# Optimization experiments

Hardware: AMD Instinct MI355X
Metric: run time of the kernel (lower is better)

## Reference

```python
import jax, jax.numpy as jnp
import numpy as np

B, N, T, C, H, HH, ED, HOR, OC = 16, 307, 12, 2, 64, 64, 8, 12, 1


def setup_inputs() -> dict:
    key = jax.random.key(0)
    ks = jax.random.split(key, 23)
    r = lambda i, shape: jax.random.normal(ks[i], shape, dtype=jnp.float32) * 0.1
    return dict(
        coeff_a=r(0, (B, N, T - 1, C)), coeff_b=r(1, (B, N, T - 1, C)),
        coeff_c=r(2, (B, N, T - 1, C)), coeff_d=r(3, (B, N, T - 1, C)),
        times=jnp.arange(T, dtype=jnp.float32),
        h_W=r(4, (C, H)), h_b=r(5, (H,)),
        z_W=r(6, (C, H)), z_b=r(7, (H,)),
        f_W_in=r(8, (H, HH)), f_b_in=r(9, (HH,)),
        f_W_mid=r(10, (HH, HH)), f_b_mid=r(11, (HH,)),
        f_W_out=r(12, (HH, H * C)), f_b_out=r(13, (H * C,)),
        g_W_in=r(14, (H, HH)), g_b_in=r(15, (HH,)),
        g_E=r(16, (N, ED)), g_Wpool=r(17, (ED, 2, HH, HH)), g_bpool=r(18, (ED, HH)),
        g_W_out=r(19, (HH, H * H)), g_b_out=r(20, (H * H,)),
        conv_W=r(21, (HOR * OC, H)), conv_b=r(22, (HOR * OC,)),
    )


def _forward(coeff_a, coeff_b, coeff_c, coeff_d, times,
             h_W, h_b, z_W, z_b,
             f_W_in, f_b_in, f_W_mid, f_b_mid, f_W_out, f_b_out,
             g_W_in, g_b_in, g_E, g_Wpool, g_bpool, g_W_out, g_b_out,
             conv_W, conv_b):
    n_int = times.shape[0] - 1

    def spline_deriv(t):
        # natural cubic spline derivative: b + (two_c + three_d*frac)*frac on interval idx
        idx = jnp.clip(jnp.searchsorted(times, t, side='right') - 1, 0, n_int - 1)
        frac = t - times[idx]
        bb = jnp.take(coeff_b, idx, axis=2)
        cc = jnp.take(coeff_c, idx, axis=2)
        dd = jnp.take(coeff_d, idx, axis=2)
        return bb + (cc + dd * frac) * frac  # (B,N,C)

    def func_f(h):
        x = jax.nn.relu(h @ f_W_in + f_b_in)
        x = jax.nn.relu(x @ f_W_mid + f_b_mid)
        x = (x @ f_W_out + f_b_out).reshape(*x.shape[:-1], H, C)
        return jnp.tanh(x)  # (B,N,H,C)

    # adaptive adjacency (constant across time, depends only on node embeddings)
    A = jax.nn.softmax(jax.nn.relu(g_E @ g_E.T), axis=1)       # (N,N)
    supports = jnp.stack([jnp.eye(N, dtype=A.dtype), A])       # (K=2,N,N)
    agc_W = jnp.einsum('nd,dkio->nkio', g_E, g_Wpool)          # (N,K,HH,HH)
    agc_b = g_E @ g_bpool                                      # (N,HH)

    def func_g(z):
        x = jax.nn.relu(z @ g_W_in + g_b_in)                   # (B,N,HH)
        x_g = jnp.einsum('knm,bmc->bnkc', supports, x)         # (B,N,K,HH)
        x = jnp.einsum('bnki,nkio->bno', x_g, agc_W) + agc_b   # (B,N,HH)
        x = jax.nn.relu(x)
        x = (x @ g_W_out + g_b_out).reshape(*x.shape[:-1], H, H)
        return jnp.tanh(x)  # (B,N,H,H)

    def vf(t, h, z):
        dX = spline_deriv(t)                                   # (B,N,C)
        f_v = func_f(h)                                        # (B,N,H,C)
        g_v = func_g(z)                                        # (B,N,H,H)
        dh = jnp.einsum('bnhc,bnc->bnh', f_v, dX)
        fg = jnp.einsum('bnij,bnjc->bnic', g_v, f_v)           # (B,N,H,C)
        dz = jnp.einsum('bnhc,bnc->bnh', fg, dX)
        return dh, dz

    # initial states from spline value at times[0] (= coeff_a at interval 0, frac 0)
    x0 = coeff_a[:, :, 0, :]                                   # (B,N,C)
    h0 = x0 @ h_W + h_b
    z0 = x0 @ z_W + z_b

    def step(carry, ts):
        h, z = carry
        t0, t1 = ts
        dt = t1 - t0
        k1h, k1z = vf(t0, h, z)
        k2h, k2z = vf(t0 + dt / 2, h + dt / 2 * k1h, z + dt / 2 * k1z)
        k3h, k3z = vf(t0 + dt / 2, h + dt / 2 * k2h, z + dt / 2 * k2z)
        k4h, k4z = vf(t1, h + dt * k3h, z + dt * k3z)
        h = h + dt / 6 * (k1h + 2 * k2h + 2 * k3h + k4h)
        z = z + dt / 6 * (k1z + 2 * k2z + 2 * k3z + k4z)
        return (h, z), None

    (hT, zT), _ = jax.lax.scan(step, (h0, z0), (times[:-1], times[1:]))

    # end_conv: Conv2d(1, HOR*OC, kernel=(1,H)) over (B,1,N,H) == linear over H
    out = jnp.einsum('bnh,oh->bon', zT, conv_W) + conv_b[None, :, None]  # (B,HOR*OC,N)
    out = out.reshape(B, HOR, OC, N).transpose(0, 1, 3, 2)               # (B,HOR,N,OC)
    return out


def reference(coeff_a, coeff_b, coeff_c, coeff_d, times,
              h_W, h_b, z_W, z_b,
              f_W_in, f_b_in, f_W_mid, f_b_mid, f_W_out, f_b_out,
              g_W_in, g_b_in, g_E, g_Wpool, g_bpool, g_W_out, g_b_out,
              conv_W, conv_b):
    return _forward(coeff_a, coeff_b, coeff_c, coeff_d, times,
                    h_W, h_b, z_W, z_b,
                    f_W_in, f_b_in, f_W_mid, f_b_mid, f_W_out, f_b_out,
                    g_W_in, g_b_in, g_E, g_Wpool, g_bpool, g_W_out, g_b_out,
                    conv_W, conv_b)
```

## Files before the change

kernel.cpp:

```cpp
#include <hip/hip_runtime.h>

#define NB 16
#define NN 307
#define NI 11

typedef __attribute__((ext_vector_type(8))) short bf16x8;
typedef __attribute__((ext_vector_type(4))) float f32x4;

#define OFF_ABF    0u
#define OFF_AGCWT  51200u
#define OFF_AGCB   1308672u
#define OFF_WT     1329152u
#define OFF_H      1460224u
#define OFF_Z      1774592u
#define OFF_KH     2088960u
#define OFF_KZ     2403328u
#define OFF_ACCH   2717696u
#define OFF_ACCZ   3032064u
#define OFF_XBF    3346432u
#define OFF_XGBF   3510272u
#define OFF_XT     3674112u
#define OFF_YBF    3837952u

__device__ __forceinline__ float tanh_fast(float x){
    float e = __expf(2.0f * x);
    return 1.0f - 2.0f * __builtin_amdgcn_rcpf(e + 1.0f);
}
__device__ __forceinline__ unsigned short f2bf(float f){
    unsigned u = __builtin_bit_cast(unsigned, f);
    unsigned r = u + 0x7FFFu + ((u >> 16) & 1u);
    return (unsigned short)(r >> 16);
}


__global__ void kA(const float* __restrict__ gE, unsigned short* __restrict__ Abf){
    int n = blockIdx.x;
    int lane = threadIdx.x;
    if (n >= NN){
#pragma unroll
        for (int ii = 0; ii < 5; ii++) Abf[n*320 + lane + 64*ii] = 0;
        return;
    }
    float en[8];
#pragma unroll
    for (int d = 0; d < 8; d++) en[d] = gE[n*8 + d];
    float vals[5];
    float mx = -1e30f;
#pragma unroll
    for (int ii = 0; ii < 5; ii++){
        int m = lane + 64*ii;
        float v = -1e30f;
        if (m < NN){
            float a = 0.f;
#pragma unroll
            for (int d = 0; d < 8; d++) a += en[d] * gE[m*8 + d];
            v = fmaxf(a, 0.f);
        }
        vals[ii] = v;
        mx = fmaxf(mx, v);
    }
#pragma unroll
    for (int off = 32; off >= 1; off >>= 1) mx = fmaxf(mx, __shfl_xor(mx, off, 64));
    float s = 0.f;
#pragma unroll
    for (int ii = 0; ii < 5; ii++){
        int m = lane + 64*ii;
        if (m < NN){ vals[ii] = __expf(vals[ii] - mx); s += vals[ii]; }
    }
#pragma unroll
    for (int off = 32; off >= 1; off >>= 1) s += __shfl_xor(s, off, 64);
    float inv = 1.f / s;
#pragma unroll
    for (int ii = 0; ii < 5; ii++){
        int m = lane + 64*ii;
        unsigned short v = 0;
        if (m < NN) v = f2bf(vals[ii] * inv);
        Abf[n*320 + m] = v;
    }
}

__global__ __launch_bounds__(256) void kAgcWT(const float* __restrict__ gE,
                                              const float* __restrict__ gWpool,
                                              unsigned short* __restrict__ agcWt){
    __shared__ float t[128*65];
    int tid = threadIdx.x;
    int n = blockIdx.x;
    float ge[8];
#pragma unroll
    for (int d = 0; d < 8; d++) ge[d] = gE[n*8 + d];
    for (int it = 0; it < 32; it++){
        int e = it*256 + tid;
        int o = e & 63, i = (e >> 6) & 63, kk = e >> 12;
        float acc = 0.f;
#pragma unroll
        for (int d = 0; d < 8; d++) acc += ge[d] * gWpool[((size_t)(d*2 + kk)*64 + i)*64 + o];
        t[(kk*64 + i)*65 + o] = acc;
    }
    __syncthreads();
    for (int it = 0; it < 32; it++){
        int e = it*256 + tid;
        int k = e & 127, o = e >> 7;
        agcWt[((size_t)n*64 + o)*128 + k] = f2bf(t[k*65 + o]);
    }
}

__global__ void kAgcB(const float* __restrict__ gE, const float* __restrict__ gbpool,
                      float* __restrict__ agcb){
    int gid = blockIdx.x*256 + threadIdx.x;
    if (gid >= NN*64) return;
    int o = gid & 63;
    int n = gid >> 6;
    float acc = 0.f;
#pragma unroll
    for (int d = 0; d < 8; d++) acc += gE[n*8 + d] * gbpool[d*64 + o];
    agcb[gid] = acc;
}

__global__ __launch_bounds__(256) void kWt(const float* __restrict__ WgOut,
                                           unsigned short* __restrict__ Wt_sw){
    __shared__ float t[64*65];
    int tid = threadIdx.x;
    int c0 = blockIdx.x*64;
    for (int it = 0; it < 16; it++){
        int e = it*256 + tid;
        int k = e >> 6, c = e & 63;
        t[k*65 + c] = WgOut[(size_t)k*4096 + c0 + c];
    }
    __syncthreads();
    for (int it = 0; it < 16; it++){
        int e = it*256 + tid;
        int c = e >> 6, k = e & 63;
        int ks = ((((k >> 3) ^ (c & 7)) << 3) | (k & 7));
        Wt_sw[(size_t)(c0 + c)*64 + ks] = f2bf(t[k*65 + c]);
    }
}

__global__ void kZeroTail(unsigned short* __restrict__ xT){
    int gid = blockIdx.x*256 + threadIdx.x;
    int mo = gid & 15, c = (gid >> 4) & 63, b = gid >> 10;
    xT[((size_t)b*64 + c)*320 + 304 + mo] = 0;
}

__global__ void kInit(const float* __restrict__ ca,
                      const float* __restrict__ hW, const float* __restrict__ hb,
                      const float* __restrict__ zW, const float* __restrict__ zb,
                      float* __restrict__ h, float* __restrict__ z){
    int gid = blockIdx.x*256 + threadIdx.x;
    int t = gid & 63;
    int bn = gid >> 6;
    float x0 = ca[bn*NI*2 + 0];
    float x1 = ca[bn*NI*2 + 1];
    h[gid] = x0*hW[t] + x1*hW[64 + t] + hb[t];
    z[gid] = x0*zW[t] + x1*zW[64 + t] + zb[t];
}

__global__ __launch_bounds__(256) void K1(
    float* __restrict__ h, const float* __restrict__ z,
    float* __restrict__ kh, const float* __restrict__ kz,
    float* __restrict__ acch, unsigned short* __restrict__ xbf,
    unsigned short* __restrict__ xT,
    const float* __restrict__ Cb, const float* __restrict__ Cc, const float* __restrict__ Cd,
    const float* __restrict__ WfIn, const float* __restrict__ fbIn,
    const float* __restrict__ WfMid, const float* __restrict__ fbMid,
    const float* __restrict__ WfOut, const float* __restrict__ fbOut,
    const float* __restrict__ WgIn, const float* __restrict__ gbIn,
    int stage, float acoef, int idx, float frac)
{
    __shared__ float4 bufA[4][16];
    __shared__ float4 bufB[4][16];
    __shared__ float4 bufZ[4][16];
    int tid = threadIdx.x;
    int wv = tid >> 6;
    int lane = tid & 63;
    int bn = blockIdx.x*4 + wv;
    int base = bn*64 + lane;
    unsigned ub = (unsigned)bn / 307u;
    int b = (int)ub;
    int n = bn - b*307;

    float hv = h[base];
    float zv = z[base];
    float sih = hv, siz = zv;
    if (stage > 0){ sih += acoef * kh[base]; siz += acoef * kz[base]; }
    ((float*)&bufA[wv][0])[lane] = sih;
    ((float*)&bufZ[wv][0])[lane] = siz;

    float a0 = fbIn[lane], a1 = 0.f, a2 = 0.f, a3 = 0.f;
#pragma unroll
    for (int k4 = 0; k4 < 16; k4 += 2){
        float4 s4 = bufA[wv][k4];
        float4 s5 = bufA[wv][k4+1];
        int k = k4*4;
        a0 += s4.x*WfIn[(k+0)*64 + lane];
        a1 += s4.y*WfIn[(k+1)*64 + lane];
        a2 += s4.z*WfIn[(k+2)*64 + lane];
        a3 += s4.w*WfIn[(k+3)*64 + lane];
        a0 += s5.x*WfIn[(k+4)*64 + lane];
        a1 += s5.y*WfIn[(k+5)*64 + lane];
        a2 += s5.z*WfIn[(k+6)*64 + lane];
        a3 += s5.w*WfIn[(k+7)*64 + lane];
    }
    float u = fmaxf((a0 + a1) + (a2 + a3), 0.f);
    ((float*)&bufB[wv][0])[lane] = u;

    float c0_ = fbMid[lane], c1_ = 0.f, c2_ = 0.f, c3_ = 0.f;
#pragma unroll
    for (int k4 = 0; k4 < 16; k4 += 2){
        float4 s4 = bufB[wv][k4];
        float4 s5 = bufB[wv][k4+1];
        int k = k4*4;
        c0_ += s4.x*WfMid[(k+0)*64 + lane];
        c1_ += s4.y*WfMid[(k+1)*64 + lane];
        c2_ += s4.z*WfMid[(k+2)*64 + lane];
        c3_ += s4.w*WfMid[(k+3)*64 + lane];
        c0_ += s5.x*WfMid[(k+4)*64 + lane];
        c1_ += s5.y*WfMid[(k+5)*64 + lane];
        c2_ += s5.z*WfMid[(k+6)*64 + lane];
        c3_ += s5.w*WfMid[(k+7)*64 + lane];
    }
    float u2v = fmaxf((c0_ + c1_) + (c2_ + c3_), 0.f);
    ((float*)&bufA[wv][0])[lane] = u2v;

    float f0a = fbOut[lane*2 + 0], f0b = 0.f;
    float f1a = fbOut[lane*2 + 1], f1b = 0.f;
    float xa = gbIn[lane], xb = 0.f;
#pragma unroll
    for (int k4 = 0; k4 < 16; k4 += 2){
        float4 s4 = bufA[wv][k4];
        float4 z4 = bufZ[wv][k4];
        float4 s5 = bufA[wv][k4+1];
        float4 z5 = bufZ[wv][k4+1];
        int k = k4*4;
        f0a += s4.x*WfOut[(k+0)*128 + lane*2+0]; f1a += s4.x*WfOut[(k+0)*128 + lane*2+1];
        f0b += s4.y*WfOut[(k+1)*128 + lane*2+0]; f1b += s4.y*WfOut[(k+1)*128 + lane*2+1];
        f0a += s4.z*WfOut[(k+2)*128 + lane*2+0]; f1a += s4.z*WfOut[(k+2)*128 + lane*2+1];
        f0b += s4.w*WfOut[(k+3)*128 + lane*2+0]; f1b += s4.w*WfOut[(k+3)*128 + lane*2+1];
        f0a += s5.x*WfOut[(k+4)*128 + lane*2+0]; f1a += s5.x*WfOut[(k+4)*128 + lane*2+1];
        f0b += s5.y*WfOut[(k+5)*128 + lane*2+0]; f1b += s5.y*WfOut[(k+5)*128 + lane*2+1];
        f0a += s5.z*WfOut[(k+6)*128 + lane*2+0]; f1a += s5.z*WfOut[(k+6)*128 + lane*2+1];
        f0b += s5.w*WfOut[(k+7)*128 + lane*2+0]; f1b += s5.w*WfOut[(k+7)*128 + lane*2+1];
        xa += z4.x*WgIn[(k+0)*64 + lane];
        xb += z4.y*WgIn[(k+1)*64 + lane];
        xa += z4.z*WgIn[(k+2)*64 + lane];
        xb += z4.w*WgIn[(k+3)*64 + lane];
        xa += z5.x*WgIn[(k+4)*64 + lane];
        xb += z5.y*WgIn[(k+5)*64 + lane];
        xa += z5.z*WgIn[(k+6)*64 + lane];
        xb += z5.w*WgIn[(k+7)*64 + lane];
    }
    float f0 = tanh_fast(f0a + f0b);
    float f1 = tanh_fast(f1a + f1b);
    float xv = fmaxf(xa + xb, 0.f);

    int cb = (bn*NI + idx)*2;
    float b0 = Cb[cb], b1 = Cb[cb+1];
    float c0 = Cc[cb], c1 = Cc[cb+1];
    float d0 = Cd[cb], d1 = Cd[cb+1];
    float dx0 = b0 + (c0 + d0*frac)*frac;
    float dx1 = b1 + (c1 + d1*frac)*frac;

    float khv = f0*dx0 + f1*dx1;
    kh[base] = khv;
    if (stage == 0)      acch[base] = khv;
    else if (stage < 3)  acch[base] += 2.f*khv;
    else                 h[base] = hv + (1.f/6.f)*(acch[base] + khv);

    unsigned short xbfv = f2bf(xv);
    xbf[((size_t)n*16 + b)*64 + lane] = xbfv;
    xT[((size_t)b*64 + lane)*320 + n] = xbfv;
}

__global__ __launch_bounds__(256) void KXG(
    const unsigned short* __restrict__ xT, const unsigned short* __restrict__ Abf,
    unsigned short* __restrict__ xgbf)
{
    int tid = threadIdx.x, lane = tid & 63, wv = tid >> 6;
    int quad = lane >> 4, l15 = lane & 15;
    int b = blockIdx.x / 20, nt = blockIdx.x % 20;
    int n0 = nt*16;

    f32x4 acc = {0.f,0.f,0.f,0.f};
#pragma unroll
    for (int mt = 0; mt < 10; mt++){
        bf16x8 a  = *(const bf16x8*)(Abf + (size_t)(n0 + l15)*320 + mt*32 + quad*8);
        bf16x8 bb = *(const bf16x8*)(xT + ((size_t)b*64 + wv*16 + l15)*320 + mt*32 + quad*8);
        acc = __builtin_amdgcn_mfma_f32_16x16x32_bf16(a, bb, acc, 0, 0, 0);
    }
#pragma unroll
    for (int r = 0; r < 4; r++){
        int n = n0 + quad*4 + r;
        xgbf[((size_t)n*16 + b)*64 + wv*16 + l15] = f2bf(acc[r]);
    }
}

__global__ __launch_bounds__(256) void KY(
    const unsigned short* __restrict__ xbf, const unsigned short* __restrict__ xgbf,
    const unsigned short* __restrict__ agcWt, const float* __restrict__ agcb,
    unsigned short* __restrict__ Ybf_g)
{
    int tid = threadIdx.x, lane = tid & 63, wv = tid >> 6;
    int quad = lane >> 4, l15 = lane & 15;
    int nw = blockIdx.x*4 + wv;
    if (nw >= NN) return;
    const size_t xrow = ((size_t)nw*16 + l15)*64;
    bf16x8 a[4];
    a[0] = *(const bf16x8*)(xbf  + xrow + 0  + quad*8);
    a[1] = *(const bf16x8*)(xbf  + xrow + 32 + quad*8);
    a[2] = *(const bf16x8*)(xgbf + xrow + 0  + quad*8);
    a[3] = *(const bf16x8*)(xgbf + xrow + 32 + quad*8);
#pragma unroll
    for (int ot = 0; ot < 4; ot++){
        f32x4 acc = {0.f,0.f,0.f,0.f};
#pragma unroll
        for (int kt = 0; kt < 4; kt++){
            bf16x8 bbb = *(const bf16x8*)(agcWt + ((size_t)nw*64 + ot*16 + l15)*128 + kt*32 + quad*8);
            acc = __builtin_amdgcn_mfma_f32_16x16x32_bf16(a[kt], bbb, acc, 0, 0, 0);
        }
        float gb = agcb[nw*64 + ot*16 + l15];
#pragma unroll
        for (int r = 0; r < 4; r++)
            Ybf_g[((size_t)nw*16 + quad*4 + r)*64 + ot*16 + l15] = f2bf(fmaxf(acc[r] + gb, 0.f));
    }
}

__global__ __launch_bounds__(256, 4) void K2g(
    float* __restrict__ z, const float* __restrict__ kh,
    float* __restrict__ kz, float* __restrict__ accz,
    const unsigned short* __restrict__ Ybf_g,
    const unsigned short* __restrict__ Wt_sw, const float* __restrict__ gbOut,
    int stage)
{
    __shared__ unsigned short WtL[256*64];
    __shared__ float dzl[4*16*5];
    int tid = threadIdx.x, lane = tid & 63, wv = tid >> 6;
    int quad = lane >> 4, l15 = lane & 15;
    int nt = blockIdx.x >> 4, cg = blockIdx.x & 15;
    int n0 = nt*4;
    int nw = n0 + wv;
    int n = nw < NN ? nw : NN-1;
    int C0 = cg*256;

#pragma unroll
    for (int it = 0; it < 8; it++){
        int seg = it*256 + wv*64 + lane;
        const unsigned short* src = Wt_sw + (size_t)C0*64 + (size_t)seg*8;
        __builtin_amdgcn_global_load_lds(
            (const __attribute__((address_space(1))) void*)src,
            (__attribute__((address_space(3))) void*)(WtL + (it*256 + wv*64)*8),
            16, 0, 0);
    }

    float4 khr[4];
#pragma unroll
    for (int c = 0; c < 4; c++)
        khr[c] = *(const float4*)(kh + ((size_t)l15*NN + n)*64 + c*16 + quad*4);
    bf16x8 bb0 = *(const bf16x8*)(Ybf_g + ((size_t)n*16 + l15)*64 + 0  + quad*8);
    bf16x8 bb1 = *(const bf16x8*)(Ybf_g + ((size_t)n*16 + l15)*64 + 32 + quad*8);

    __syncthreads();

    int sw = l15 & 7;
#pragma unroll
    for (int i4 = 0; i4 < 4; i4++){
        float pacc = 0.f;
#pragma unroll
        for (int c4 = 0; c4 < 4; c4++){
            int ct = i4*4 + c4;
            int row = ct*16 + l15;
            f32x4 acc = {0.f,0.f,0.f,0.f};
            bf16x8 a0 = *(const bf16x8*)(WtL + row*64 + (((quad)     ^ sw) << 3));
            acc = __builtin_amdgcn_mfma_f32_16x16x32_bf16(a0, bb0, acc, 0, 0, 0);
            bf16x8 a1 = *(const bf16x8*)(WtL + row*64 + (((4 + quad) ^ sw) << 3));
            acc = __builtin_amdgcn_mfma_f32_16x16x32_bf16(a1, bb1, acc, 0, 0, 0);
            float4 gb4 = *(const float4*)(gbOut + C0 + ct*16 + quad*4);
            float4 kh4 = khr[c4];
            pacc += tanh_fast(acc[0] + gb4.x) * kh4.x
                  + tanh_fast(acc[1] + gb4.y) * kh4.y
                  + tanh_fast(acc[2] + gb4.z) * kh4.z
                  + tanh_fast(acc[3] + gb4.w) * kh4.w;
        }
        pacc += __shfl_xor(pacc, 16, 64);
        pacc += __shfl_xor(pacc, 32, 64);
        if (quad == 0) dzl[(wv*16 + l15)*5 + i4] = pacc;
    }

    {
        int w = tid >> 6, bb_ = (tid >> 2) & 15, il = tid & 3;
        int nn = n0 + w;
        if (nn < NN){
            size_t addr = ((size_t)bb_*NN + nn)*64 + cg*4 + il;
            float v = dzl[(w*16 + bb_)*5 + il];
            kz[addr] = v;
            if (stage == 0)      accz[addr] = v;
            else if (stage < 3)  accz[addr] += 2.f*v;
            else                 z[addr] += (1.f/6.f)*(accz[addr] + v);
        }
    }
}

__global__ __launch_bounds__(256) void kOut(const float* __restrict__ z,
                                            const float* __restrict__ convW,
                                            const float* __restrict__ convB,
                                            float* __restrict__ out){
    int gid = blockIdx.x*256 + threadIdx.x;
    if (gid >= NB*NN) return;
    int b = gid / NN, n = gid % NN;
    float zr[64];
    const float4* zp = (const float4*)(z + (size_t)gid*64);
#pragma unroll
    for (int k4 = 0; k4 < 16; k4++){
        float4 v = zp[k4];
        zr[k4*4+0] = v.x; zr[k4*4+1] = v.y; zr[k4*4+2] = v.z; zr[k4*4+3] = v.w;
    }
#pragma unroll
    for (int o = 0; o < 12; o++){
        float acc = convB[o];
#pragma unroll
        for (int hh = 0; hh < 64; hh++) acc += zr[hh]*convW[o*64 + hh];
        out[(b*12 + o)*NN + n] = acc;
    }
}

extern "C" void kernel_launch(void* const* d_in, const int* in_sizes, int n_in,
                              void* d_out, int out_size, void* d_ws, size_t ws_size,
                              hipStream_t stream)
{
    const float* coeff_a = (const float*)d_in[0];
    const float* coeff_b = (const float*)d_in[1];
    const float* coeff_c = (const float*)d_in[2];
    const float* coeff_d = (const float*)d_in[3];
    const float* hW     = (const float*)d_in[5];
    const float* hb     = (const float*)d_in[6];
    const float* zW     = (const float*)d_in[7];
    const float* zb     = (const float*)d_in[8];
    const float* WfIn   = (const float*)d_in[9];
    const float* fbIn   = (const float*)d_in[10];
    const float* WfMid  = (const float*)d_in[11];
    const float* fbMid  = (const float*)d_in[12];
    const float* WfOut  = (const float*)d_in[13];
    const float* fbOut  = (const float*)d_in[14];
    const float* WgIn   = (const float*)d_in[15];
    const float* gbIn   = (const float*)d_in[16];
    const float* gE     = (const float*)d_in[17];
    const float* gWpool = (const float*)d_in[18];
    const float* gbpool = (const float*)d_in[19];
    const float* WgOut  = (const float*)d_in[20];
    const float* gbOut  = (const float*)d_in[21];
    const float* convW  = (const float*)d_in[22];
    const float* convB  = (const float*)d_in[23];

    float* ws = (float*)d_ws;
    unsigned short* Abf   = (unsigned short*)(ws + OFF_ABF);
    unsigned short* agcWt = (unsigned short*)(ws + OFF_AGCWT);
    float*          agcb  = ws + OFF_AGCB;
    unsigned short* Wt_sw = (unsigned short*)(ws + OFF_WT);
    float* h    = ws + OFF_H;
    float* z    = ws + OFF_Z;
    float* kh   = ws + OFF_KH;
    float* kz   = ws + OFF_KZ;
    float* acch = ws + OFF_ACCH;
    float* accz = ws + OFF_ACCZ;
    unsigned short* xbf  = (unsigned short*)(ws + OFF_XBF);
    unsigned short* xgbf = (unsigned short*)(ws + OFF_XGBF);
    unsigned short* xT   = (unsigned short*)(ws + OFF_XT);
    unsigned short* Ybf  = (unsigned short*)(ws + OFF_YBF);
    float* out = (float*)d_out;

    kA        <<<320, 64,  0, stream>>>(gE, Abf);
    kAgcWT    <<<NN,  256, 0, stream>>>(gE, gWpool, agcWt);
    kAgcB     <<<77,  256, 0, stream>>>(gE, gbpool, agcb);
    kWt       <<<64,  256, 0, stream>>>(WgOut, Wt_sw);
    kZeroTail <<<64,  256, 0, stream>>>(xT);
    kInit     <<<1228,256, 0, stream>>>(coeff_a, hW, hb, zW, zb, h, z);

    const float acoef[4] = {0.f, 0.5f, 0.5f, 1.f};
    for (int step = 0; step < 11; step++){
        for (int s = 0; s < 4; s++){
            int idx; float frac;
            if (s == 0)      { idx = step;     frac = 0.f;  }
            else if (s < 3)  { idx = step;     frac = 0.5f; }
            else if (step<10){ idx = step + 1; frac = 0.f;  }
            else             { idx = 10;       frac = 1.f;  }
            K1 <<<1228, 256, 0, stream>>>(h, z, kh, kz, acch, xbf, xT,
                coeff_b, coeff_c, coeff_d, WfIn, fbIn, WfMid, fbMid,
                WfOut, fbOut, WgIn, gbIn, s, acoef[s], idx, frac);
            KXG<<<320, 256, 0, stream>>>(xT, Abf, xgbf);
            KY <<<77,  256, 0, stream>>>(xbf, xgbf, agcWt, agcb, Ybf);
            K2g<<<1232, 256, 0, stream>>>(z, kh, kz, accz, Ybf,
                Wt_sw, gbOut, s);
        }
    }
    kOut<<<20, 256, 0, stream>>>(z, convW, convB, out);
}
```

Measured before the change: 2.266 ms.

## Fuse per-node AGC projection into K2g and process two node sets per block

```diff
diff --git a/kernel.cpp b/kernel.cpp
--- a/kernel.cpp
+++ b/kernel.cpp
@@ -20,7 +20,6 @@
 #define OFF_XBF    3346432u
 #define OFF_XGBF   3510272u
 #define OFF_XT     3674112u
-#define OFF_YBF    3837952u
 
 __device__ __forceinline__ float tanh_fast(float x){
     float e = __expf(2.0f * x);
@@ -293,51 +292,21 @@
     }
 }
 
-__global__ __launch_bounds__(256) void KY(
+__global__ __launch_bounds__(256, 3) void K2g(
+    float* __restrict__ z, const float* __restrict__ kh,
+    float* __restrict__ kz, float* __restrict__ accz,
     const unsigned short* __restrict__ xbf, const unsigned short* __restrict__ xgbf,
     const unsigned short* __restrict__ agcWt, const float* __restrict__ agcb,
-    unsigned short* __restrict__ Ybf_g)
-{
-    int tid = threadIdx.x, lane = tid & 63, wv = tid >> 6;
-    int quad = lane >> 4, l15 = lane & 15;
-    int nw = blockIdx.x*4 + wv;
-    if (nw >= NN) return;
-    const size_t xrow = ((size_t)nw*16 + l15)*64;
-    bf16x8 a[4];
-    a[0] = *(const bf16x8*)(xbf  + xrow + 0  + quad*8);
-    a[1] = *(const bf16x8*)(xbf  + xrow + 32 + quad*8);
-    a[2] = *(const bf16x8*)(xgbf + xrow + 0  + quad*8);
-    a[3] = *(const bf16x8*)(xgbf + xrow + 32 + quad*8);
-#pragma unroll
-    for (int ot = 0; ot < 4; ot++){
-        f32x4 acc = {0.f,0.f,0.f,0.f};
-#pragma unroll
-        for (int kt = 0; kt < 4; kt++){
-            bf16x8 bbb = *(const bf16x8*)(agcWt + ((size_t)nw*64 + ot*16 + l15)*128 + kt*32 + quad*8);
-            acc = __builtin_amdgcn_mfma_f32_16x16x32_bf16(a[kt], bbb, acc, 0, 0, 0);
-        }
-        float gb = agcb[nw*64 + ot*16 + l15];
-#pragma unroll
-        for (int r = 0; r < 4; r++)
-            Ybf_g[((size_t)nw*16 + quad*4 + r)*64 + ot*16 + l15] = f2bf(fmaxf(acc[r] + gb, 0.f));
-    }
-}
-
-__global__ __launch_bounds__(256, 4) void K2g(
-    float* __restrict__ z, const float* __restrict__ kh,
-    float* __restrict__ kz, float* __restrict__ accz,
-    const unsigned short* __restrict__ Ybf_g,
     const unsigned short* __restrict__ Wt_sw, const float* __restrict__ gbOut,
     int stage)
 {
     __shared__ unsigned short WtL[256*64];
-    __shared__ float dzl[4*16*5];
+    __shared__ unsigned short Ybf[128*68];
+    __shared__ float dzl[8*16*5];
     int tid = threadIdx.x, lane = tid & 63, wv = tid >> 6;
     int quad = lane >> 4, l15 = lane & 15;
     int nt = blockIdx.x >> 4, cg = blockIdx.x & 15;
-    int n0 = nt*4;
-    int nw = n0 + wv;
-    int n = nw < NN ? nw : NN-1;
+    int n0 = nt*8;
     int C0 = cg*256;
 
 #pragma unroll
@@ -350,42 +319,90 @@
             16, 0, 0);
     }
 
-    float4 khr[4];
-#pragma unroll
-    for (int c = 0; c < 4; c++)
-        khr[c] = *(const float4*)(kh + ((size_t)l15*NN + n)*64 + c*16 + quad*4);
-    bf16x8 bb0 = *(const bf16x8*)(Ybf_g + ((size_t)n*16 + l15)*64 + 0  + quad*8);
-    bf16x8 bb1 = *(const bf16x8*)(Ybf_g + ((size_t)n*16 + l15)*64 + 32 + quad*8);
+    int nA = min(n0 + wv,     NN-1);
+    int nB = min(n0 + 4 + wv, NN-1);
+
+    float4 khrA[4], khrB[4];
+#pragma unroll
+    for (int c = 0; c < 4; c++){
+        khrA[c] = *(const float4*)(kh + ((size_t)l15*NN + nA)*64 + c*16 + quad*4);
+        khrB[c] = *(const float4*)(kh + ((size_t)l15*NN + nB)*64 + c*16 + quad*4);
+    }
+
+#pragma unroll
+    for (int set = 0; set < 2; set++){
+        int n = set ? nB : nA;
+        const size_t xrow = ((size_t)n*16 + l15)*64;
+        bf16x8 a[4];
+        a[0] = *(const bf16x8*)(xbf  + xrow + 0  + quad*8);
+        a[1] = *(const bf16x8*)(xbf  + xrow + 32 + quad*8);
+        a[2] = *(const bf16x8*)(xgbf + xrow + 0  + quad*8);
+        a[3] = *(const bf16x8*)(xgbf + xrow + 32 + quad*8);
+#pragma unroll
+        for (int ot = 0; ot < 4; ot++){
+            f32x4 acc = {0.f,0.f,0.f,0.f};
+#pragma unroll
+            for (int kt = 0; kt < 4; kt++){
+                bf16x8 bbb = *(const bf16x8*)(agcWt + ((size_t)n*64 + ot*16 + l15)*128 + kt*32 + quad*8);
+                acc = __builtin_amdgcn_mfma_f32_16x16x32_bf16(a[kt], bbb, acc, 0, 0, 0);
+            }
+            float gb = agcb[n*64 + ot*16 + l15];
+#pragma unroll
+            for (int r = 0; r < 4; r++)
+                Ybf[((set*4 + wv)*16 + quad*4 + r)*68 + ot*16 + l15] =
+                    f2bf(fmaxf(acc[r] + gb, 0.f));
+        }
+    }
 
     __syncthreads();
 
+    bf16x8 bbA0 = *(const bf16x8*)(Ybf + ((0*4 + wv)*16 + l15)*68 + 0  + quad*8);
+    bf16x8 bbA1 = *(const bf16x8*)(Ybf + ((0*4 + wv)*16 + l15)*68 + 32 + quad*8);
+    bf16x8 bbB0 = *(const bf16x8*)(Ybf + ((1*4 + wv)*16 + l15)*68 + 0  + quad*8);
+    bf16x8 bbB1 = *(const bf16x8*)(Ybf + ((1*4 + wv)*16 + l15)*68 + 32 + quad*8);
+
     int sw = l15 & 7;
 #pragma unroll
     for (int i4 = 0; i4 < 4; i4++){
-        float pacc = 0.f;
+        float pA = 0.f, pB = 0.f;
 #pragma unroll
         for (int c4 = 0; c4 < 4; c4++){
             int ct = i4*4 + c4;
             int row = ct*16 + l15;
-            f32x4 acc = {0.f,0.f,0.f,0.f};
             bf16x8 a0 = *(const bf16x8*)(WtL + row*64 + (((quad)     ^ sw) << 3));
-            acc = __builtin_amdgcn_mfma_f32_16x16x32_bf16(a0, bb0, acc, 0, 0, 0);
             bf16x8 a1 = *(const bf16x8*)(WtL + row*64 + (((4 + quad) ^ sw) << 3));
-            acc = __builtin_amdgcn_mfma_f32_16x16x32_bf16(a1, bb1, acc, 0, 0, 0);
+            f32x4 accA = {0.f,0.f,0.f,0.f};
+            accA = __builtin_amdgcn_mfma_f32_16x16x32_bf16(a0, bbA0, accA, 0, 0, 0);
+            accA = __builtin_amdgcn_mfma_f32_16x16x32_bf16(a1, bbA1, accA, 0, 0, 0);
+            f32x4 accB = {0.f,0.f,0.f,0.f};
+            accB = __builtin_amdgcn_mfma_f32_16x16x32_bf16(a0, bbB0, accB, 0, 0, 0);
+            accB = __builtin_amdgcn_mfma_f32_16x16x32_bf16(a1, bbB1, accB, 0, 0, 0);
             float4 gb4 = *(const float4*)(gbOut + C0 + ct*16 + quad*4);
-            float4 kh4 = khr[c4];
-            pacc += tanh_fast(acc[0] + gb4.x) * kh4.x
-                  + tanh_fast(acc[1] + gb4.y) * kh4.y
-                  + tanh_fast(acc[2] + gb4.z) * kh4.z
-                  + tanh_fast(acc[3] + gb4.w) * kh4.w;
+            float4 kA4 = khrA[c4];
+            float4 kB4 = khrB[c4];
+            pA += tanh_fast(accA[0] + gb4.x) * kA4.x
+                + tanh_fast(accA[1] + gb4.y) * kA4.y
+                + tanh_fast(accA[2] + gb4.z) * kA4.z
+                + tanh_fast(accA[3] + gb4.w) * kA4.w;
+            pB += tanh_fast(accB[0] + gb4.x) * kB4.x
+                + tanh_fast(accB[1] + gb4.y) * kB4.y
+                + tanh_fast(accB[2] + gb4.z) * kB4.z
+                + tanh_fast(accB[3] + gb4.w) * kB4.w;
         }
-        pacc += __shfl_xor(pacc, 16, 64);
-        pacc += __shfl_xor(pacc, 32, 64);
-        if (quad == 0) dzl[(wv*16 + l15)*5 + i4] = pacc;
-    }
-
-    {
-        int w = tid >> 6, bb_ = (tid >> 2) & 15, il = tid & 3;
+        pA += __shfl_xor(pA, 16, 64);
+        pA += __shfl_xor(pA, 32, 64);
+        pB += __shfl_xor(pB, 16, 64);
+        pB += __shfl_xor(pB, 32, 64);
+        if (quad == 0){
+            dzl[((0*4 + wv)*16 + l15)*5 + i4] = pA;
+            dzl[((1*4 + wv)*16 + l15)*5 + i4] = pB;
+        }
+    }
+
+#pragma unroll
+    for (int it = 0; it < 2; it++){
+        int e = it*256 + tid;
+        int w = e >> 6, bb_ = (e >> 2) & 15, il = e & 3;
         int nn = n0 + w;
         if (nn < NN){
             size_t addr = ((size_t)bb_*NN + nn)*64 + cg*4 + il;
@@ -463,7 +480,6 @@
     unsigned short* xbf  = (unsigned short*)(ws + OFF_XBF);
     unsigned short* xgbf = (unsigned short*)(ws + OFF_XGBF);
     unsigned short* xT   = (unsigned short*)(ws + OFF_XT);
-    unsigned short* Ybf  = (unsigned short*)(ws + OFF_YBF);
     float* out = (float*)d_out;
 
     kA        <<<320, 64,  0, stream>>>(gE, Abf);
@@ -485,9 +501,8 @@
                 coeff_b, coeff_c, coeff_d, WfIn, fbIn, WfMid, fbMid,
                 WfOut, fbOut, WgIn, gbIn, s, acoef[s], idx, frac);
             KXG<<<320, 256, 0, stream>>>(xT, Abf, xgbf);
-            KY <<<77,  256, 0, stream>>>(xbf, xgbf, agcWt, agcb, Ybf);
-            K2g<<<1232, 256, 0, stream>>>(z, kh, kz, accz, Ybf,
-                Wt_sw, gbOut, s);
+            K2g<<<624, 256, 0, stream>>>(z, kh, kz, accz, xbf, xgbf,
+                agcWt, agcb, Wt_sw, gbOut, s);
         }
     }
     kOut<<<20, 256, 0, stream>>>(z, convW, convB, out);
```

Result: slower. 2.543 ms (+12.2%).

## Precompute h-trajectory in one persistent kernel and fuse KY into K2

Applied to the files above, without the earlier changes.

```diff
diff --git a/kernel.cpp b/kernel.cpp
--- a/kernel.cpp
+++ b/kernel.cpp
@@ -13,14 +13,14 @@
 #define OFF_WT     1329152u
 #define OFF_H      1460224u
 #define OFF_Z      1774592u
-#define OFF_KH     2088960u
-#define OFF_KZ     2403328u
-#define OFF_ACCH   2717696u
-#define OFF_ACCZ   3032064u
-#define OFF_XBF    3346432u
-#define OFF_XGBF   3510272u
-#define OFF_XT     3674112u
-#define OFF_YBF    3837952u
+#define OFF_KZ     2088960u
+#define OFF_ACCZ   2403328u
+#define OFF_XBF    2717696u
+#define OFF_XGBF   2881536u
+#define OFF_XT     3045376u
+#define OFF_KHALL  3209216u
+
+#define STG_STRIDE 314368u
 
 __device__ __forceinline__ float tanh_fast(float x){
     float e = __expf(2.0f * x);
@@ -154,91 +154,133 @@
     z[gid] = x0*zW[t] + x1*zW[64 + t] + zb[t];
 }
 
-__global__ __launch_bounds__(256) void K1(
-    float* __restrict__ h, const float* __restrict__ z,
-    float* __restrict__ kh, const float* __restrict__ kz,
-    float* __restrict__ acch, unsigned short* __restrict__ xbf,
-    unsigned short* __restrict__ xT,
+__global__ __launch_bounds__(256) void KH(
+    const float* __restrict__ h0, float* __restrict__ khAll,
     const float* __restrict__ Cb, const float* __restrict__ Cc, const float* __restrict__ Cd,
     const float* __restrict__ WfIn, const float* __restrict__ fbIn,
     const float* __restrict__ WfMid, const float* __restrict__ fbMid,
-    const float* __restrict__ WfOut, const float* __restrict__ fbOut,
-    const float* __restrict__ WgIn, const float* __restrict__ gbIn,
-    int stage, float acoef, int idx, float frac)
+    const float* __restrict__ WfOut, const float* __restrict__ fbOut)
 {
     __shared__ float4 bufA[4][16];
     __shared__ float4 bufB[4][16];
+    int tid = threadIdx.x;
+    int wv = tid >> 6;
+    int lane = tid & 63;
+    int bn = blockIdx.x*4 + wv;
+    int base = bn*64 + lane;
+
+    float hv = h0[base];
+    float acch = 0.f, khprev = 0.f;
+
+#pragma unroll 1
+    for (int stage = 0; stage < 44; stage++){
+        int step = stage >> 2, s = stage & 3;
+        float acoef = (s == 0) ? 0.f : (s == 3 ? 1.f : 0.5f);
+        int idx; float frac;
+        if (s == 0)        { idx = step;     frac = 0.f;  }
+        else if (s < 3)    { idx = step;     frac = 0.5f; }
+        else if (step < 10){ idx = step + 1; frac = 0.f;  }
+        else               { idx = 10;       frac = 1.f;  }
+
+        float sih = hv + acoef * khprev;
+        ((float*)&bufA[wv][0])[lane] = sih;
+
+        float a0 = fbIn[lane], a1 = 0.f, a2 = 0.f, a3 = 0.f;
+#pragma unroll
+        for (int k4 = 0; k4 < 16; k4 += 2){
+            float4 s4 = bufA[wv][k4];
+            float4 s5 = bufA[wv][k4+1];
+            int k = k4*4;
+            a0 += s4.x*WfIn[(k+0)*64 + lane];
+            a1 += s4.y*WfIn[(k+1)*64 + lane];
+            a2 += s4.z*WfIn[(k+2)*64 + lane];
+            a3 += s4.w*WfIn[(k+3)*64 + lane];
+            a0 += s5.x*WfIn[(k+4)*64 + lane];
+            a1 += s5.y*WfIn[(k+5)*64 + lane];
+            a2 += s5.z*WfIn[(k+6)*64 + lane];
+            a3 += s5.w*WfIn[(k+7)*64 + lane];
+        }
+        float u = fmaxf((a0 + a1) + (a2 + a3), 0.f);
+        ((float*)&bufB[wv][0])[lane] = u;
+
+        float c0_ = fbMid[lane], c1_ = 0.f, c2_ = 0.f, c3_ = 0.f;
+#pragma unroll
+        for (int k4 = 0; k4 < 16; k4 += 2){
+            float4 s4 = bufB[wv][k4];
+            float4 s5 = bufB[wv][k4+1];
+            int k = k4*4;
+            c0_ += s4.x*WfMid[(k+0)*64 + lane];
+            c1_ += s4.y*WfMid[(k+1)*64 + lane];
+            c2_ += s4.z*WfMid[(k+2)*64 + lane];
+            c3_ += s4.w*WfMid[(k+3)*64 + lane];
+            c0_ += s5.x*WfMid[(k+4)*64 + lane];
+            c1_ += s5.y*WfMid[(k+5)*64 + lane];
+            c2_ += s5.z*WfMid[(k+6)*64 + lane];
+            c3_ += s5.w*WfMid[(k+7)*64 + lane];
+        }
+        float u2v = fmaxf((c0_ + c1_) + (c2_ + c3_), 0.f);
+        ((float*)&bufA[wv][0])[lane] = u2v;
+
+        float f0a = fbOut[lane*2 + 0], f0b = 0.f;
+        float f1a = fbOut[lane*2 + 1], f1b = 0.f;
+#pragma unroll
+        for (int k4 = 0; k4 < 16; k4 += 2){
+            float4 s4 = bufA[wv][k4];
+            float4 s5 = bufA[wv][k4+1];
+            int k = k4*4;
+            f0a += s4.x*WfOut[(k+0)*128 + lane*2+0]; f1a += s4.x*WfOut[(k+0)*128 + lane*2+1];
+            f0b += s4.y*WfOut[(k+1)*128 + lane*2+0]; f1b += s4.y*WfOut[(k+1)*128 + lane*2+1];
+            f0a += s4.z*WfOut[(k+2)*128 + lane*2+0]; f1a += s4.z*WfOut[(k+2)*128 + lane*2+1];
+            f0b += s4.w*WfOut[(k+3)*128 + lane*2+0]; f1b += s4.w*WfOut[(k+3)*128 + lane*2+1];
+            f0a += s5.x*WfOut[(k+4)*128 + lane*2+0]; f1a += s5.x*WfOut[(k+4)*128 + lane*2+1];
+            f0b += s5.y*WfOut[(k+5)*128 + lane*2+0]; f1b += s5.y*WfOut[(k+5)*128 + lane*2+1];
+            f0a += s5.z*WfOut[(k+6)*128 + lane*2+0]; f1a += s5.z*WfOut[(k+6)*128 + lane*2+1];
+            f0b += s5.w*WfOut[(k+7)*128 + lane*2+0]; f1b += s5.w*WfOut[(k+7)*128 + lane*2+1];
+        }
+        float f0 = tanh_fast(f0a + f0b);
+        float f1 = tanh_fast(f1a + f1b);
+
+        int cb = (bn*NI + idx)*2;
+        float b0 = Cb[cb], b1 = Cb[cb+1];
+        float c0 = Cc[cb], c1 = Cc[cb+1];
+        float d0 = Cd[cb], d1 = Cd[cb+1];
+        float dx0 = b0 + (c0 + d0*frac)*frac;
+        float dx1 = b1 + (c1 + d1*frac)*frac;
+
+        float khv = f0*dx0 + f1*dx1;
+        khAll[(size_t)stage*STG_STRIDE + base] = khv;
+        if (s == 0)      acch = khv;
+        else if (s < 3)  acch += 2.f*khv;
+        else             hv = hv + (1.f/6.f)*(acch + khv);
+        khprev = khv;
+    }
+}
+
+__global__ __launch_bounds__(256) void Kz1(
+    const float* __restrict__ z, const float* __restrict__ kz,
+    unsigned short* __restrict__ xbf, unsigned short* __restrict__ xT,
+    const float* __restrict__ WgIn, const float* __restrict__ gbIn,
+    int stage, float acoef)
+{
     __shared__ float4 bufZ[4][16];
     int tid = threadIdx.x;
     int wv = tid >> 6;
     int lane = tid & 63;
     int bn = blockIdx.x*4 + wv;
     int base = bn*64 + lane;
-    unsigned ub = (unsigned)bn / 307u;
-    int b = (int)ub;
+    int b = (int)((unsigned)bn / 307u);
     int n = bn - b*307;
 
-    float hv = h[base];
-    float zv = z[base];
-    float sih = hv, siz = zv;
-    if (stage > 0){ sih += acoef * kh[base]; siz += acoef * kz[base]; }
-    ((float*)&bufA[wv][0])[lane] = sih;
+    float siz = z[base];
+    if (stage > 0) siz += acoef * kz[base];
     ((float*)&bufZ[wv][0])[lane] = siz;
 
-    float a0 = fbIn[lane], a1 = 0.f, a2 = 0.f, a3 = 0.f;
+    float xa = gbIn[lane], xb = 0.f;
 #pragma unroll
     for (int k4 = 0; k4 < 16; k4 += 2){
-        float4 s4 = bufA[wv][k4];
-        float4 s5 = bufA[wv][k4+1];
-        int k = k4*4;
-        a0 += s4.x*WfIn[(k+0)*64 + lane];
-        a1 += s4.y*WfIn[(k+1)*64 + lane];
-        a2 += s4.z*WfIn[(k+2)*64 + lane];
-        a3 += s4.w*WfIn[(k+3)*64 + lane];
-        a0 += s5.x*WfIn[(k+4)*64 + lane];
-        a1 += s5.y*WfIn[(k+5)*64 + lane];
-        a2 += s5.z*WfIn[(k+6)*64 + lane];
-        a3 += s5.w*WfIn[(k+7)*64 + lane];
-    }
-    float u = fmaxf((a0 + a1) + (a2 + a3), 0.f);
-    ((float*)&bufB[wv][0])[lane] = u;
-
-    float c0_ = fbMid[lane], c1_ = 0.f, c2_ = 0.f, c3_ = 0.f;
-#pragma unroll
-    for (int k4 = 0; k4 < 16; k4 += 2){
-        float4 s4 = bufB[wv][k4];
-        float4 s5 = bufB[wv][k4+1];
-        int k = k4*4;
-        c0_ += s4.x*WfMid[(k+0)*64 + lane];
-        c1_ += s4.y*WfMid[(k+1)*64 + lane];
-        c2_ += s4.z*WfMid[(k+2)*64 + lane];
-        c3_ += s4.w*WfMid[(k+3)*64 + lane];
-        c0_ += s5.x*WfMid[(k+4)*64 + lane];
-        c1_ += s5.y*WfMid[(k+5)*64 + lane];
-        c2_ += s5.z*WfMid[(k+6)*64 + lane];
-        c3_ += s5.w*WfMid[(k+7)*64 + lane];
-    }
-    float u2v = fmaxf((c0_ + c1_) + (c2_ + c3_), 0.f);
-    ((float*)&bufA[wv][0])[lane] = u2v;
-
-    float f0a = fbOut[lane*2 + 0], f0b = 0.f;
-    float f1a = fbOut[lane*2 + 1], f1b = 0.f;
-    float xa = gbIn[lane], xb = 0.f;
-#pragma unroll
-    for (int k4 = 0; k4 < 16; k4 += 2){
-        float4 s4 = bufA[wv][k4];
         float4 z4 = bufZ[wv][k4];
-        float4 s5 = bufA[wv][k4+1];
         float4 z5 = bufZ[wv][k4+1];
         int k = k4*4;
-        f0a += s4.x*WfOut[(k+0)*128 + lane*2+0]; f1a += s4.x*WfOut[(k+0)*128 + lane*2+1];
-        f0b += s4.y*WfOut[(k+1)*128 + lane*2+0]; f1b += s4.y*WfOut[(k+1)*128 + lane*2+1];
-        f0a += s4.z*WfOut[(k+2)*128 + lane*2+0]; f1a += s4.z*WfOut[(k+2)*128 + lane*2+1];
-        f0b += s4.w*WfOut[(k+3)*128 + lane*2+0]; f1b += s4.w*WfOut[(k+3)*128 + lane*2+1];
-        f0a += s5.x*WfOut[(k+4)*128 + lane*2+0]; f1a += s5.x*WfOut[(k+4)*128 + lane*2+1];
-        f0b += s5.y*WfOut[(k+5)*128 + lane*2+0]; f1b += s5.y*WfOut[(k+5)*128 + lane*2+1];
-        f0a += s5.z*WfOut[(k+6)*128 + lane*2+0]; f1a += s5.z*WfOut[(k+6)*128 + lane*2+1];
-        f0b += s5.w*WfOut[(k+7)*128 + lane*2+0]; f1b += s5.w*WfOut[(k+7)*128 + lane*2+1];
         xa += z4.x*WgIn[(k+0)*64 + lane];
         xb += z4.y*WgIn[(k+1)*64 + lane];
         xa += z4.z*WgIn[(k+2)*64 + lane];
@@ -248,24 +290,7 @@
         xa += z5.z*WgIn[(k+6)*64 + lane];
         xb += z5.w*WgIn[(k+7)*64 + lane];
     }
-    float f0 = tanh_fast(f0a + f0b);
-    float f1 = tanh_fast(f1a + f1b);
-    float xv = fmaxf(xa + xb, 0.f);
-
-    int cb = (bn*NI + idx)*2;
-    float b0 = Cb[cb], b1 = Cb[cb+1];
-    float c0 = Cc[cb], c1 = Cc[cb+1];
-    float d0 = Cd[cb], d1 = Cd[cb+1];
-    float dx0 = b0 + (c0 + d0*frac)*frac;
-    float dx1 = b1 + (c1 + d1*frac)*frac;
-
-    float khv = f0*dx0 + f1*dx1;
-    kh[base] = khv;
-    if (stage == 0)      acch[base] = khv;
-    else if (stage < 3)  acch[base] += 2.f*khv;
-    else                 h[base] = hv + (1.f/6.f)*(acch[base] + khv);
-
-    unsigned short xbfv = f2bf(xv);
+    unsigned short xbfv = f2bf(fmaxf(xa + xb, 0.f));
     xbf[((size_t)n*16 + b)*64 + lane] = xbfv;
     xT[((size_t)b*64 + lane)*320 + n] = xbfv;
 }
@@ -293,44 +318,16 @@
     }
 }
 
-__global__ __launch_bounds__(256) void KY(
+__global__ __launch_bounds__(256, 3) void K2f(
+    float* __restrict__ z, const float* __restrict__ khS,
+    float* __restrict__ kz, float* __restrict__ accz,
     const unsigned short* __restrict__ xbf, const unsigned short* __restrict__ xgbf,
     const unsigned short* __restrict__ agcWt, const float* __restrict__ agcb,
-    unsigned short* __restrict__ Ybf_g)
-{
-    int tid = threadIdx.x, lane = tid & 63, wv = tid >> 6;
-    int quad = lane >> 4, l15 = lane & 15;
-    int nw = blockIdx.x*4 + wv;
-    if (nw >= NN) return;
-    const size_t xrow = ((size_t)nw*16 + l15)*64;
-    bf16x8 a[4];
-    a[0] = *(const bf16x8*)(xbf  + xrow + 0  + quad*8);
-    a[1] = *(const bf16x8*)(xbf  + xrow + 32 + quad*8);
-    a[2] = *(const bf16x8*)(xgbf + xrow + 0  + quad*8);
-    a[3] = *(const bf16x8*)(xgbf + xrow + 32 + quad*8);
-#pragma unroll
-    for (int ot = 0; ot < 4; ot++){
-        f32x4 acc = {0.f,0.f,0.f,0.f};
-#pragma unroll
-        for (int kt = 0; kt < 4; kt++){
-            bf16x8 bbb = *(const bf16x8*)(agcWt + ((size_t)nw*64 + ot*16 + l15)*128 + kt*32 + quad*8);
-            acc = __builtin_amdgcn_mfma_f32_16x16x32_bf16(a[kt], bbb, acc, 0, 0, 0);
-        }
-        float gb = agcb[nw*64 + ot*16 + l15];
-#pragma unroll
-        for (int r = 0; r < 4; r++)
-            Ybf_g[((size_t)nw*16 + quad*4 + r)*64 + ot*16 + l15] = f2bf(fmaxf(acc[r] + gb, 0.f));
-    }
-}
-
-__global__ __launch_bounds__(256, 4) void K2g(
-    float* __restrict__ z, const float* __restrict__ kh,
-    float* __restrict__ kz, float* __restrict__ accz,
-    const unsigned short* __restrict__ Ybf_g,
     const unsigned short* __restrict__ Wt_sw, const float* __restrict__ gbOut,
     int stage)
 {
     __shared__ unsigned short WtL[256*64];
+    __shared__ unsigned short Ybf[64*68];
     __shared__ float dzl[4*16*5];
     int tid = threadIdx.x, lane = tid & 63, wv = tid >> 6;
     int quad = lane >> 4, l15 = lane & 15;
@@ -353,11 +350,34 @@
     float4 khr[4];
 #pragma unroll
     for (int c = 0; c < 4; c++)
-        khr[c] = *(const float4*)(kh + ((size_t)l15*NN + n)*64 + c*16 + quad*4);
-    bf16x8 bb0 = *(const bf16x8*)(Ybf_g + ((size_t)n*16 + l15)*64 + 0  + quad*8);
-    bf16x8 bb1 = *(const bf16x8*)(Ybf_g + ((size_t)n*16 + l15)*64 + 32 + quad*8);
+        khr[c] = *(const float4*)(khS + ((size_t)l15*NN + n)*64 + c*16 + quad*4);
+
+    {
+        const size_t xrow = ((size_t)n*16 + l15)*64;
+        bf16x8 a[4];
+        a[0] = *(const bf16x8*)(xbf  + xrow + 0  + quad*8);
+        a[1] = *(const bf16x8*)(xbf  + xrow + 32 + quad*8);
+        a[2] = *(const bf16x8*)(xgbf + xrow + 0  + quad*8);
+        a[3] = *(const bf16x8*)(xgbf + xrow + 32 + quad*8);
+#pragma unroll
+        for (int ot = 0; ot < 4; ot++){
+            f32x4 acc = {0.f,0.f,0.f,0.f};
+#pragma unroll
+            for (int kt = 0; kt < 4; kt++){
+                bf16x8 bbb = *(const bf16x8*)(agcWt + ((size_t)n*64 + ot*16 + l15)*128 + kt*32 + quad*8);
+                acc = __builtin_amdgcn_mfma_f32_16x16x32_bf16(a[kt], bbb, acc, 0, 0, 0);
+            }
+            float gb = agcb[n*64 + ot*16 + l15];
+#pragma unroll
+            for (int r = 0; r < 4; r++)
+                Ybf[(wv*16 + quad*4 + r)*68 + ot*16 + l15] = f2bf(fmaxf(acc[r] + gb, 0.f));
+        }
+    }
 
     __syncthreads();
+
+    bf16x8 bb0 = *(const bf16x8*)(Ybf + (wv*16 + l15)*68 + 0  + quad*8);
+    bf16x8 bb1 = *(const bf16x8*)(Ybf + (wv*16 + l15)*68 + 32 + quad*8);
 
     int sw = l15 & 7;
 #pragma unroll
@@ -454,16 +474,14 @@
     unsigned short* agcWt = (unsigned short*)(ws + OFF_AGCWT);
     float*          agcb  = ws + OFF_AGCB;
     unsigned short* Wt_sw = (unsigned short*)(ws + OFF_WT);
-    float* h    = ws + OFF_H;
-    float* z    = ws + OFF_Z;
-    float* kh   = ws + OFF_KH;
-    float* kz   = ws + OFF_KZ;
-    float* acch = ws + OFF_ACCH;
-    float* accz = ws + OFF_ACCZ;
+    float* h     = ws + OFF_H;
+    float* z     = ws + OFF_Z;
+    float* kz    = ws + OFF_KZ;
+    float* accz  = ws + OFF_ACCZ;
     unsigned short* xbf  = (unsigned short*)(ws + OFF_XBF);
     unsigned short* xgbf = (unsigned short*)(ws + OFF_XGBF);
     unsigned short* xT   = (unsigned short*)(ws + OFF_XT);
-    unsigned short* Ybf  = (unsigned short*)(ws + OFF_YBF);
+    float* khAll = ws + OFF_KHALL;
     float* out = (float*)d_out;
 
     kA        <<<320, 64,  0, stream>>>(gE, Abf);
@@ -473,21 +491,17 @@
     kZeroTail <<<64,  256, 0, stream>>>(xT);
     kInit     <<<1228,256, 0, stream>>>(coeff_a, hW, hb, zW, zb, h, z);
 
+    KH<<<1228, 256, 0, stream>>>(h, khAll, coeff_b, coeff_c, coeff_d,
+                                 WfIn, fbIn, WfMid, fbMid, WfOut, fbOut);
+
     const float acoef[4] = {0.f, 0.5f, 0.5f, 1.f};
     for (int step = 0; step < 11; step++){
         for (int s = 0; s < 4; s++){
-            int idx; float frac;
-            if (s == 0)      { idx = step;     frac = 0.f;  }
-            else if (s < 3)  { idx = step;     frac = 0.5f; }
-            else if (step<10){ idx = step + 1; frac = 0.f;  }
-            else             { idx = 10;       frac = 1.f;  }
-            K1 <<<1228, 256, 0, stream>>>(h, z, kh, kz, acch, xbf, xT,
-                coeff_b, coeff_c, coeff_d, WfIn, fbIn, WfMid, fbMid,
-                WfOut, fbOut, WgIn, gbIn, s, acoef[s], idx, frac);
+            const float* khS = khAll + (size_t)(step*4 + s)*STG_STRIDE;
+            Kz1<<<1228, 256, 0, stream>>>(z, kz, xbf, xT, WgIn, gbIn, s, acoef[s]);
             KXG<<<320, 256, 0, stream>>>(xT, Abf, xgbf);
-            KY <<<77,  256, 0, stream>>>(xbf, xgbf, agcWt, agcb, Ybf);
-            K2g<<<1232, 256, 0, stream>>>(z, kh, kz, accz, Ybf,
-                Wt_sw, gbOut, s);
+            K2f<<<1232, 256, 0, stream>>>(z, khS, kz, accz, xbf, xgbf,
+                                          agcWt, agcb, Wt_sw, gbOut, s);
         }
     }
     kOut<<<20, 256, 0, stream>>>(z, convW, convB, out);
```

Result: faster. 2.094 ms (-7.6%).
